# Kernel optimization log

Measured on AMD Instinct MI355X. Metric: run time of the kernel, lower is better.

Reference implementation:

```python
import jax, jax.numpy as jnp
import numpy as np

OUT_H, OUT_W = 7, 7
SPATIAL_SCALE = 0.25
SAMPLING_RATIO = 2


def setup_inputs() -> dict:
    key = jax.random.key(0)
    kf, kb, kc, ks = jax.random.split(key, 4)
    B, C, H, W = 2, 256, 200, 200
    N, IMG = 1000, 800.0
    features = jax.random.normal(kf, (B, C, H, W), jnp.float32)
    bidx = jax.random.randint(kb, (N,), 0, B).astype(jnp.float32)
    ctr = jax.random.uniform(kc, (N, 2)) * IMG            # box centers in image coords
    size = jax.random.uniform(ks, (N, 2)) * 256.0 + 16.0  # box sizes 16..272 px
    x1y1 = jnp.clip(ctr - size / 2, 0.0, IMG)
    x2y2 = jnp.clip(ctr + size / 2, 0.0, IMG)
    rois = jnp.concatenate(
        [bidx[:, None], x1y1[:, 0:1], x1y1[:, 1:2], x2y2[:, 0:1], x2y2[:, 1:2]], axis=1
    )
    return {"features": features, "rois": rois}


def _roi_align(features, rois):
    # torchvision.ops.roi_align semantics (aligned=False), fully vectorized over ROIs.
    B, C, H, W = features.shape
    N = rois.shape[0]
    ph, pw, ratio, scale = OUT_H, OUT_W, SAMPLING_RATIO, SPATIAL_SCALE
    b = rois[:, 0].astype(jnp.int32)
    x1, y1, x2, y2 = (rois[:, i] * scale for i in (1, 2, 3, 4))
    roi_w = jnp.maximum(x2 - x1, 1.0)
    roi_h = jnp.maximum(y2 - y1, 1.0)
    bin_w = roi_w / pw
    bin_h = roi_h / ph
    # sample coordinate s within bin p: y1 + (p*ratio + i + 0.5) * bin_h / ratio
    sy = jnp.arange(ph * ratio, dtype=features.dtype)
    sx = jnp.arange(pw * ratio, dtype=features.dtype)
    y = y1[:, None] + (sy[None, :] + 0.5) * (bin_h[:, None] / ratio)  # (N, Sy)
    x = x1[:, None] + (sx[None, :] + 0.5) * (bin_w[:, None] / ratio)  # (N, Sx)
    valid = ((y >= -1.0) & (y <= float(H)))[:, :, None] & \
            ((x >= -1.0) & (x <= float(W)))[:, None, :]               # (N, Sy, Sx)
    yc = jnp.clip(y, 0.0, H - 1.0)
    xc = jnp.clip(x, 0.0, W - 1.0)
    y0 = jnp.floor(yc).astype(jnp.int32)
    x0 = jnp.floor(xc).astype(jnp.int32)
    y1i = jnp.minimum(y0 + 1, H - 1)
    x1i = jnp.minimum(x0 + 1, W - 1)
    ly = (yc - y0)[:, :, None, None]  # (N, Sy, 1, 1)
    lx = (xc - x0)[:, None, :, None]  # (N, 1, Sx, 1)
    hy, hx = 1.0 - ly, 1.0 - lx

    def gather(yi, xi):
        # advanced indexing -> (N, Sy, Sx, C)
        return features[b[:, None, None], :, yi[:, :, None], xi[:, None, :]]

    val = (hy * hx * gather(y0, x0) + hy * lx * gather(y0, x1i)
           + ly * hx * gather(y1i, x0) + ly * lx * gather(y1i, x1i))
    val = jnp.where(valid[..., None], val, 0.0)
    val = val.reshape(N, ph, ratio, pw, ratio, C).mean(axis=(2, 4))  # avg sampling points
    return val.transpose(0, 3, 1, 2)  # (N, C, ph, pw)


def reference(features, rois):
    return _roi_align(features, rois)
```

## Files before the change

kernel.cpp:

```cpp
#include <hip/hip_runtime.h>
#include <hip/hip_fp16.h>

#define OUT_H 7
#define OUT_W 7
#define NPOS  49
#define RATIO 2
#define SCALE 0.25f
#define CCH 256
#define FH 200
#define FW 200
#define FHW (FH * FW)
#define LROW 65

struct __align__(16) H8 { __half2 h[4]; };

__device__ __forceinline__ void acc8(float (&a)[8], const H8& v, float w) {
    #pragma unroll
    for (int k = 0; k < 4; ++k) {
        a[2*k]   = fmaf(__low2float(v.h[k]),  w, a[2*k]);
        a[2*k+1] = fmaf(__high2float(v.h[k]), w, a[2*k+1]);
    }
}

__global__ __launch_bounds__(256) void transpose_cp(
    const float* __restrict__ in, __half* __restrict__ outT)
{
    int bid = blockIdx.x;
    int pt   = bid % 625;
    int rest = bid / 625;
    int ct   = rest & 3;
    int b    = rest >> 2;

    __shared__ unsigned short tile[64][66];
    int tid = threadIdx.x;
    int pix0 = pt * 64, c0 = ct * 64;
    int xl = tid & 63;

    const float* src = in + ((size_t)b * CCH + c0) * FHW + pix0;
    #pragma unroll
    for (int k = 0; k < 16; ++k) {
        int cl = (tid >> 6) + 4 * k;
        tile[xl][cl] = __half_as_ushort(__float2half(src[(size_t)cl * FHW + xl]));
    }
    __syncthreads();

    __half* dst = outT + ((size_t)b * FHW + pix0) * CCH + c0;
    #pragma unroll
    for (int j = 0; j < 8; ++j) {
        int idx = tid + 256 * j;
        int pl = idx >> 5;
        int cp = idx & 31;
        *(unsigned int*)((char*)dst + (size_t)pl * (CCH * 2) + 4 * cp) =
            *(const unsigned int*)&tile[pl][2 * cp];
    }
}

__global__ __launch_bounds__(256, 4) void roi_gather_v9(
    const __half* __restrict__ featT,
    const float* __restrict__ rois,
    float* __restrict__ out,
    int N)
{
    int bid = blockIdx.x;
    int n  = bid >> 2;
    int cq = bid & 3;
    int tid = threadIdx.x;
    int wave = tid >> 6, lane = tid & 63;
    int g = lane >> 3;
    int l = lane & 7;

    __shared__ float lds[NPOS * LROW];

    const float* r = rois + (size_t)n * 5;
    int   b  = (int)r[0];
    float x1 = r[1] * SCALE, y1 = r[2] * SCALE;
    float roi_w = fmaxf(r[3] * SCALE - x1, 1.0f);
    float roi_h = fmaxf(r[4] * SCALE - y1, 1.0f);
    float step_x = roi_w * (1.0f / (OUT_W * RATIO));
    float step_y = roi_h * (1.0f / (OUT_H * RATIO));

    const char* base = (const char*)featT + (size_t)b * ((size_t)FHW * CCH * 2);
    const uint32_t laneoff = (uint32_t)(cq * 64 + l * 8) * 2;

    #pragma unroll 1
    for (int rnd = 0; rnd < 2; ++rnd) {
        int p = rnd * 32 + wave * 8 + g;
        if (p < NPOS) {
            int ph = p / OUT_W;
            int pw = p - ph * OUT_W;

            uint32_t o00[4], dxx[4], rst[4];
            float w[4][4];
            #pragma unroll
            for (int iy = 0; iy < RATIO; ++iy) {
                float yy = y1 + ((float)(ph * RATIO + iy) + 0.5f) * step_y;
                bool  vy = (yy >= -1.0f) && (yy <= (float)FH);
                float yc = fminf(fmaxf(yy, 0.0f), (float)(FH - 1));
                int   yi0 = (int)yc;
                float ly = yc - (float)yi0, hy = 1.0f - ly;
                uint32_t row0  = (uint32_t)yi0 * (FW * CCH * 2);
                uint32_t rstep = (yi0 < FH - 1) ? (FW * CCH * 2) : 0u;
                #pragma unroll
                for (int ix = 0; ix < RATIO; ++ix) {
                    int s = iy * RATIO + ix;
                    float xx = x1 + ((float)(pw * RATIO + ix) + 0.5f) * step_x;
                    bool  vx = (xx >= -1.0f) && (xx <= (float)FW);
                    float xc = fminf(fmaxf(xx, 0.0f), (float)(FW - 1));
                    int   xi0 = (int)xc;
                    float lx = xc - (float)xi0, hx = 1.0f - lx;
                    float vm  = (vy && vx) ? 0.25f : 0.0f;
                    float hyv = hy * vm, lyv = ly * vm;
                    o00[s] = row0 + (uint32_t)xi0 * (CCH * 2) + laneoff;
                    dxx[s] = (xi0 < FW - 1) ? (CCH * 2) : 0u;
                    rst[s] = rstep;
                    w[s][0] = hyv * hx; w[s][1] = hyv * lx;
                    w[s][2] = lyv * hx; w[s][3] = lyv * lx;
                }
            }

            H8 v[16];
            #pragma unroll
            for (int s = 0; s < 4; ++s) {
                v[4*s+0] = *(const H8*)(base + o00[s]);
                v[4*s+1] = *(const H8*)(base + o00[s] + dxx[s]);
                v[4*s+2] = *(const H8*)(base + o00[s] + rst[s]);
                v[4*s+3] = *(const H8*)(base + o00[s] + rst[s] + dxx[s]);
            }
            __builtin_amdgcn_sched_barrier(0);

            float acc[8];
            #pragma unroll
            for (int k = 0; k < 8; ++k) acc[k] = 0.0f;
            #pragma unroll
            for (int s = 0; s < 4; ++s) {
                #pragma unroll
                for (int c4 = 0; c4 < 4; ++c4)
                    acc8(acc, v[4*s+c4], w[s][c4]);
            }

            float* lp = &lds[p * LROW + l * 8];
            #pragma unroll
            for (int k = 0; k < 8; ++k) lp[k] = acc[k];
        }
    }
    __syncthreads();

    float* oblk = out + ((size_t)n * CCH + cq * 64) * NPOS;
    #pragma unroll 1
    for (int o = tid; o < 64 * NPOS; o += 256) {
        int c = o / NPOS;
        int p = o - c * NPOS;
        __builtin_nontemporal_store(lds[p * LROW + c], &oblk[o]);
    }
}

__global__ __launch_bounds__(256) void roi_align_kernel(
    const float* __restrict__ feat, const float* __restrict__ rois,
    float* __restrict__ out, int N, int C, int H, int W)
{
    int idx = blockIdx.x * blockDim.x + threadIdx.x;
    int total = N * C * OUT_H * OUT_W;
    if (idx >= total) return;
    int pw = idx % OUT_W;
    int ph = (idx / OUT_W) % OUT_H;
    int c  = (idx / (OUT_W * OUT_H)) % C;
    int n  = idx / (OUT_W * OUT_H * C);
    const float* r = rois + (size_t)n * 5;
    int   b  = (int)r[0];
    float x1 = r[1] * SCALE, y1 = r[2] * SCALE;
    float roi_w = fmaxf(r[3] * SCALE - x1, 1.0f);
    float roi_h = fmaxf(r[4] * SCALE - y1, 1.0f);
    float step_y = roi_h * (1.0f / (OUT_H * RATIO));
    float step_x = roi_w * (1.0f / (OUT_W * RATIO));
    const float* fptr = feat + ((size_t)b * C + c) * (size_t)(H * W);
    float acc = 0.0f;
    #pragma unroll
    for (int iy = 0; iy < RATIO; ++iy) {
        float y = y1 + ((float)(ph * RATIO + iy) + 0.5f) * step_y;
        bool vy = (y >= -1.0f) && (y <= (float)H);
        float ycl = fminf(fmaxf(y, 0.0f), (float)(H - 1));
        int y0 = (int)floorf(ycl), y1i = min(y0 + 1, H - 1);
        float ly = ycl - (float)y0, hy = 1.0f - ly;
        #pragma unroll
        for (int ix = 0; ix < RATIO; ++ix) {
            float x = x1 + ((float)(pw * RATIO + ix) + 0.5f) * step_x;
            bool vx = (x >= -1.0f) && (x <= (float)W);
            float xcl = fminf(fmaxf(x, 0.0f), (float)(W - 1));
            int x0 = (int)floorf(xcl), x1i = min(x0 + 1, W - 1);
            float lx = xcl - (float)x0, hx = 1.0f - lx;
            const float* row0 = fptr + (size_t)y0 * W;
            const float* row1 = fptr + (size_t)y1i * W;
            float v = hy * hx * row0[x0] + hy * lx * row0[x1i]
                    + ly * hx * row1[x0] + ly * lx * row1[x1i];
            acc += (vy && vx) ? v : 0.0f;
        }
    }
    out[idx] = acc * (1.0f / (RATIO * RATIO));
}

extern "C" void kernel_launch(void* const* d_in, const int* in_sizes, int n_in,
                              void* d_out, int out_size, void* d_ws, size_t ws_size,
                              hipStream_t stream) {
    const float* feat = (const float*)d_in[0];
    const float* rois = (const float*)d_in[1];
    float* out = (float*)d_out;

    const int N = in_sizes[1] / 5;
    const int B = in_sizes[0] / (CCH * FHW);

    size_t need = (size_t)B * FHW * CCH * sizeof(__half);
    if (ws_size >= need) {
        __half* featT = (__half*)d_ws;
        transpose_cp<<<B * 4 * 625, 256, 0, stream>>>(feat, featT);
        roi_gather_v9<<<4 * N, 256, 0, stream>>>(featT, rois, out, N);
    } else {
        int total = N * CCH * OUT_H * OUT_W;
        roi_align_kernel<<<(total + 255) / 256, 256, 0, stream>>>(
            feat, rois, out, N, CCH, FH, FW);
    }
}
```

Measured before the change: 60.25 us.

## Restructure ROI gather to one block per ROI with full-channel waves

The gather kernel now launches one 512-thread block per ROI instead of four 256-thread blocks per ROI, each covering a channel quarter. Each wave handles one output bin at a time across all 256 channels, with each lane loading 8-byte half4 vectors, and two bins are processed per iteration so more loads are in flight. The LDS tile is resized to hold all channels, and the writeback de-interleaves the lane-major channel layout. This cuts the redundant per-block ROI coordinate math and gives fully coalesced 512-byte pixel reads per wave, at the cost of fewer, larger blocks and more serialized sample iterations per wave. An unused placeholder lambda is left in the code.

```diff
diff --git a/kernel.cpp b/kernel.cpp
--- a/kernel.cpp
+++ b/kernel.cpp
@@ -10,17 +10,10 @@
 #define FH 200
 #define FW 200
 #define FHW (FH * FW)
-#define LROW 65
-
-struct __align__(16) H8 { __half2 h[4]; };
-
-__device__ __forceinline__ void acc8(float (&a)[8], const H8& v, float w) {
-    #pragma unroll
-    for (int k = 0; k < 4; ++k) {
-        a[2*k]   = fmaf(__low2float(v.h[k]),  w, a[2*k]);
-        a[2*k+1] = fmaf(__high2float(v.h[k]), w, a[2*k+1]);
-    }
-}
+#define LROW 257
+#define PIXB (CCH * 2)
+
+struct __align__(8) H4 { __half2 a, b; };
 
 __global__ __launch_bounds__(256) void transpose_cp(
     const float* __restrict__ in, __half* __restrict__ outT)
@@ -55,21 +48,18 @@
     }
 }
 
-__global__ __launch_bounds__(256, 4) void roi_gather_v9(
+__global__ __launch_bounds__(512) void roi_gather_v10(
     const __half* __restrict__ featT,
     const float* __restrict__ rois,
     float* __restrict__ out,
     int N)
 {
-    int bid = blockIdx.x;
-    int n  = bid >> 2;
-    int cq = bid & 3;
+    int n   = blockIdx.x;
     int tid = threadIdx.x;
-    int wave = tid >> 6, lane = tid & 63;
-    int g = lane >> 3;
-    int l = lane & 7;
-
-    __shared__ float lds[NPOS * LROW];
+    int wv   = tid >> 6;
+    int lane = tid & 63;
+
+    __shared__ float lds[50 * LROW];
 
     const float* r = rois + (size_t)n * 5;
     int   b  = (int)r[0];
@@ -79,78 +69,117 @@
     float step_x = roi_w * (1.0f / (OUT_W * RATIO));
     float step_y = roi_h * (1.0f / (OUT_H * RATIO));
 
-    const char* base = (const char*)featT + (size_t)b * ((size_t)FHW * CCH * 2);
-    const uint32_t laneoff = (uint32_t)(cq * 64 + l * 8) * 2;
+    const char* base = (const char*)featT + (size_t)b * ((size_t)FHW * PIXB);
+    const uint32_t loff = (uint32_t)lane * 8;
+
+    auto prep = [&](int p, uint32_t (&addr)[4], float (&wt)[4]) {
+        int ph = p / OUT_W;
+        int pw = p - ph * OUT_W;
+        bool pv = (p < NPOS);
+        (void)pv; (void)ph; (void)pw; (void)addr; (void)wt;
+    };
+    (void)prep;
 
     #pragma unroll 1
-    for (int rnd = 0; rnd < 2; ++rnd) {
-        int p = rnd * 32 + wave * 8 + g;
-        if (p < NPOS) {
-            int ph = p / OUT_W;
-            int pw = p - ph * OUT_W;
-
-            uint32_t o00[4], dxx[4], rst[4];
-            float w[4][4];
+    for (int ii = 0; ii < 7; ii += 2) {
+        int p1 = ii * 8 + wv;
+        int p2 = p1 + 8;
+        int sp1 = (p1 < NPOS) ? p1 : NPOS;
+        int sp2 = (p2 < NPOS) ? p2 : NPOS;
+
+        float acc1[4] = {0.f, 0.f, 0.f, 0.f};
+        float acc2[4] = {0.f, 0.f, 0.f, 0.f};
+
+        #pragma unroll
+        for (int iy = 0; iy < RATIO; ++iy) {
             #pragma unroll
-            for (int iy = 0; iy < RATIO; ++iy) {
-                float yy = y1 + ((float)(ph * RATIO + iy) + 0.5f) * step_y;
-                bool  vy = (yy >= -1.0f) && (yy <= (float)FH);
-                float yc = fminf(fmaxf(yy, 0.0f), (float)(FH - 1));
-                int   yi0 = (int)yc;
-                float ly = yc - (float)yi0, hy = 1.0f - ly;
-                uint32_t row0  = (uint32_t)yi0 * (FW * CCH * 2);
-                uint32_t rstep = (yi0 < FH - 1) ? (FW * CCH * 2) : 0u;
-                #pragma unroll
-                for (int ix = 0; ix < RATIO; ++ix) {
-                    int s = iy * RATIO + ix;
+            for (int ix = 0; ix < RATIO; ++ix) {
+                uint32_t a1[4]; float w1[4];
+                {
+                    int ph = p1 / OUT_W, pw = p1 - (p1 / OUT_W) * OUT_W;
+                    float yy = y1 + ((float)(ph * RATIO + iy) + 0.5f) * step_y;
                     float xx = x1 + ((float)(pw * RATIO + ix) + 0.5f) * step_x;
-                    bool  vx = (xx >= -1.0f) && (xx <= (float)FW);
+                    bool  vv = (p1 < NPOS) && (yy >= -1.0f) && (yy <= (float)FH)
+                                          && (xx >= -1.0f) && (xx <= (float)FW);
+                    float yc = fminf(fmaxf(yy, 0.0f), (float)(FH - 1));
                     float xc = fminf(fmaxf(xx, 0.0f), (float)(FW - 1));
-                    int   xi0 = (int)xc;
+                    int yi0 = (int)yc, xi0 = (int)xc;
+                    float ly = yc - (float)yi0, hy = 1.0f - ly;
                     float lx = xc - (float)xi0, hx = 1.0f - lx;
-                    float vm  = (vy && vx) ? 0.25f : 0.0f;
-                    float hyv = hy * vm, lyv = ly * vm;
-                    o00[s] = row0 + (uint32_t)xi0 * (CCH * 2) + laneoff;
-                    dxx[s] = (xi0 < FW - 1) ? (CCH * 2) : 0u;
-                    rst[s] = rstep;
-                    w[s][0] = hyv * hx; w[s][1] = hyv * lx;
-                    w[s][2] = lyv * hx; w[s][3] = lyv * lx;
+                    uint32_t rw = (uint32_t)(yi0 * FW + xi0) * PIXB;
+                    uint32_t dx = (xi0 < FW - 1) ? PIXB : 0u;
+                    uint32_t dy = (yi0 < FH - 1) ? (FW * PIXB) : 0u;
+                    a1[0] = rw;        a1[1] = rw + dx;
+                    a1[2] = rw + dy;   a1[3] = rw + dy + dx;
+                    float vm = vv ? 0.25f : 0.0f;
+                    w1[0] = hy * hx * vm; w1[1] = hy * lx * vm;
+                    w1[2] = ly * hx * vm; w1[3] = ly * lx * vm;
+                }
+                uint32_t a2[4]; float w2[4];
+                {
+                    int ph = p2 / OUT_W, pw = p2 - (p2 / OUT_W) * OUT_W;
+                    float yy = y1 + ((float)(ph * RATIO + iy) + 0.5f) * step_y;
+                    float xx = x1 + ((float)(pw * RATIO + ix) + 0.5f) * step_x;
+                    bool  vv = (p2 < NPOS) && (yy >= -1.0f) && (yy <= (float)FH)
+                                          && (xx >= -1.0f) && (xx <= (float)FW);
+                    float yc = fminf(fmaxf(yy, 0.0f), (float)(FH - 1));
+                    float xc = fminf(fmaxf(xx, 0.0f), (float)(FW - 1));
+                    int yi0 = (int)yc, xi0 = (int)xc;
+                    float ly = yc - (float)yi0, hy = 1.0f - ly;
+                    float lx = xc - (float)xi0, hx = 1.0f - lx;
+                    uint32_t rw = (uint32_t)(yi0 * FW + xi0) * PIXB;
+                    uint32_t dx = (xi0 < FW - 1) ? PIXB : 0u;
+                    uint32_t dy = (yi0 < FH - 1) ? (FW * PIXB) : 0u;
+                    a2[0] = rw;        a2[1] = rw + dx;
+                    a2[2] = rw + dy;   a2[3] = rw + dy + dx;
+                    float vm = vv ? 0.25f : 0.0f;
+                    w2[0] = hy * hx * vm; w2[1] = hy * lx * vm;
+                    w2[2] = ly * hx * vm; w2[3] = ly * lx * vm;
+                }
+
+                H4 v1[4], v2[4];
+                #pragma unroll
+                for (int c4 = 0; c4 < 4; ++c4)
+                    v1[c4] = *(const H4*)(base + a1[c4] + loff);
+                #pragma unroll
+                for (int c4 = 0; c4 < 4; ++c4)
+                    v2[c4] = *(const H4*)(base + a2[c4] + loff);
+                __builtin_amdgcn_sched_barrier(0);
+
+                #pragma unroll
+                for (int c4 = 0; c4 < 4; ++c4) {
+                    float2 fa = __half22float2(v1[c4].a);
+                    float2 fb = __half22float2(v1[c4].b);
+                    acc1[0] = fmaf(fa.x, w1[c4], acc1[0]);
+                    acc1[1] = fmaf(fa.y, w1[c4], acc1[1]);
+                    acc1[2] = fmaf(fb.x, w1[c4], acc1[2]);
+                    acc1[3] = fmaf(fb.y, w1[c4], acc1[3]);
+                }
+                #pragma unroll
+                for (int c4 = 0; c4 < 4; ++c4) {
+                    float2 fa = __half22float2(v2[c4].a);
+                    float2 fb = __half22float2(v2[c4].b);
+                    acc2[0] = fmaf(fa.x, w2[c4], acc2[0]);
+                    acc2[1] = fmaf(fa.y, w2[c4], acc2[1]);
+                    acc2[2] = fmaf(fb.x, w2[c4], acc2[2]);
+                    acc2[3] = fmaf(fb.y, w2[c4], acc2[3]);
                 }
             }
-
-            H8 v[16];
-            #pragma unroll
-            for (int s = 0; s < 4; ++s) {
-                v[4*s+0] = *(const H8*)(base + o00[s]);
-                v[4*s+1] = *(const H8*)(base + o00[s] + dxx[s]);
-                v[4*s+2] = *(const H8*)(base + o00[s] + rst[s]);
-                v[4*s+3] = *(const H8*)(base + o00[s] + rst[s] + dxx[s]);
-            }
-            __builtin_amdgcn_sched_barrier(0);
-
-            float acc[8];
-            #pragma unroll
-            for (int k = 0; k < 8; ++k) acc[k] = 0.0f;
-            #pragma unroll
-            for (int s = 0; s < 4; ++s) {
-                #pragma unroll
-                for (int c4 = 0; c4 < 4; ++c4)
-                    acc8(acc, v[4*s+c4], w[s][c4]);
-            }
-
-            float* lp = &lds[p * LROW + l * 8];
-            #pragma unroll
-            for (int k = 0; k < 8; ++k) lp[k] = acc[k];
         }
+
+        #pragma unroll
+        for (int k = 0; k < 4; ++k) lds[sp1 * LROW + k * 64 + lane] = acc1[k];
+        #pragma unroll
+        for (int k = 0; k < 4; ++k) lds[sp2 * LROW + k * 64 + lane] = acc2[k];
     }
     __syncthreads();
 
-    float* oblk = out + ((size_t)n * CCH + cq * 64) * NPOS;
+    float* oblk = out + (size_t)n * (CCH * NPOS);
     #pragma unroll 1
-    for (int o = tid; o < 64 * NPOS; o += 256) {
+    for (int o = tid; o < CCH * NPOS; o += 512) {
         int c = o / NPOS;
         int p = o - c * NPOS;
-        __builtin_nontemporal_store(lds[p * LROW + c], &oblk[o]);
+        __builtin_nontemporal_store(lds[p * LROW + (c & 3) * 64 + (c >> 2)], &oblk[o]);
     }
 }
 
@@ -212,7 +241,7 @@
     if (ws_size >= need) {
         __half* featT = (__half*)d_ws;
         transpose_cp<<<B * 4 * 625, 256, 0, stream>>>(feat, featT);
-        roi_gather_v9<<<4 * N, 256, 0, stream>>>(featT, rois, out, N);
+        roi_gather_v10<<<N, 512, 0, stream>>>(featT, rois, out, N);
     } else {
         int total = N * CCH * OUT_H * OUT_W;
         roi_align_kernel<<<(total + 255) / 256, 256, 0, stream>>>(
```

After: 77.79 us. +29.1%, slower.
